# Optimization experiments

Hardware: AMD Instinct MI355X
Metric: run time of the kernel (lower is better)

Reference implementation:

```python
import jax, jax.numpy as jnp
import numpy as np

N_PTS = 500000
IN_DIM = 2
M_FOURIER = 32
J_WAVELET = 3
Q = 12
DEGREE = 3
N_CONTROL = 25
EMB_DIM = 2 * M_FOURIER + 2 * (2 ** J_WAVELET - 1)  # 78
LN_EPS = 1e-5


def make_open_uniform_knots(num_control, degree):
    n_knots = num_control + degree + 1  # 29
    if n_knots <= 2 * (degree + 1):
        return np.linspace(0.0, 1.0, n_knots).astype(np.float32)
    n_internal = n_knots - 2 * (degree + 1)
    internal = np.linspace(0.0, 1.0, n_internal + 2)[1:-1]
    return np.concatenate([np.zeros(degree + 1), internal, np.ones(degree + 1)]).astype(np.float32)

KNOTS = jnp.asarray(make_open_uniform_knots(N_CONTROL, DEGREE))


def bspline_basis(x, knots, degree, n_basis):
    # x: (M,) -> (M, n_basis); faithful (truncated) Cox-de-Boor as in source
    x = jnp.clip(x, knots[0], knots[-1])
    left = knots[:n_basis]
    right = knots[1:n_basis + 1]
    N = ((x[:, None] >= left) & (x[:, None] < right)).astype(x.dtype)
    last = ((x >= left[-1]) & (x <= right[-1])).astype(x.dtype)
    N = N.at[:, -1].set(last)
    for p in range(1, degree + 1):
        d1 = knots[p:p + n_basis] - knots[:n_basis]
        d2 = knots[p + 1:p + 1 + n_basis] - knots[1:1 + n_basis]
        c1 = jnp.where(d1 != 0, (x[:, None] - knots[:n_basis]) / jnp.where(d1 != 0, d1, 1.0), 0.0)
        c2 = jnp.where(d2 != 0, (knots[p + 1:p + 1 + n_basis] - x[:, None]) / jnp.where(d2 != 0, d2, 1.0), 0.0)
        N_shift = jnp.concatenate([N[:, 1:], jnp.zeros_like(N[:, :1])], axis=1)  # i+1 < n_basis guard
        N = c1 * N + c2 * N_shift
    return N


def wavelet_features_2d(z, J):
    x, t = z[:, 0], z[:, 1]
    feats = []
    for j in range(J):
        num_k = 2 ** j
        scale = max(0.5 / num_k, 0.001)
        centers = jnp.asarray([(k + 0.5) / num_k for k in range(num_k)], dtype=z.dtype)
        ux = x[:, None] - centers[None, :]
        ut = t[:, None] - centers[None, :]
        for u in (ux, ut):
            v = u / scale
            feats.append((1.0 - v * v) * jnp.exp(-0.5 * v * v))
    return jnp.concatenate(feats, axis=1)  # (N, 2*(2^J-1))


def setup_inputs() -> dict:
    key = jax.random.key(0)
    ks = jax.random.split(key, 6)
    xt = jax.random.uniform(ks[0], (N_PTS, IN_DIM), dtype=jnp.float32)
    B_fourier = jax.random.normal(ks[1], (M_FOURIER, IN_DIM), dtype=jnp.float32) * 1.0  # sigma_B
    ln_gamma = jnp.ones((EMB_DIM,), jnp.float32)
    ln_beta = jnp.zeros((EMB_DIM,), jnp.float32)
    W = jax.random.normal(ks[2], (Q, EMB_DIM), dtype=jnp.float32) * 0.05
    b_inner = jnp.zeros((Q,), jnp.float32)
    inner_scale = jnp.asarray(0.5, jnp.float32)
    coeffs = jax.random.normal(ks[3], (Q, N_CONTROL), dtype=jnp.float32) * 0.05
    a = jax.random.normal(ks[4], (Q, 1), dtype=jnp.float32) * 0.05
    b_out = jnp.zeros((1,), jnp.float32)
    return {"xt": xt, "B_fourier": B_fourier, "ln_gamma": ln_gamma, "ln_beta": ln_beta,
            "W": W, "b_inner": b_inner, "inner_scale": inner_scale, "coeffs": coeffs,
            "a": a, "b_out": b_out}


def reference(xt, B_fourier, ln_gamma, ln_beta, W, b_inner, inner_scale, coeffs, a, b_out):
    # Fourier features
    proj = (2.0 * np.pi) * (xt @ B_fourier.T)  # (N, M)
    scale = 1.0 / (np.sqrt(M_FOURIER) + 1e-12)
    F = jnp.concatenate([jnp.sin(proj) * scale, jnp.cos(proj) * scale], axis=1)
    # Wavelet features
    Wf = wavelet_features_2d(xt, J_WAVELET)
    emb = jnp.concatenate([F, Wf], axis=1)  # (N, 78)
    # LayerNorm
    mu = jnp.mean(emb, axis=-1, keepdims=True)
    var = jnp.mean(jnp.square(emb - mu), axis=-1, keepdims=True)
    emb = (emb - mu) / jnp.sqrt(var + LN_EPS) * ln_gamma + ln_beta
    # KAN B-spline core
    u_inner = emb @ W.T + b_inner  # (N, Q)
    s = 0.5 * (jnp.tanh(inner_scale * u_inner) + 1.0)
    B_flat = bspline_basis(s.reshape(-1), KNOTS, DEGREE, N_CONTROL)  # (N*Q, 25)
    B = B_flat.reshape(emb.shape[0], Q, N_CONTROL)
    phi = jnp.einsum('nqc,qc->nq', B, coeffs)
    u_out = phi @ a + b_out  # (N, 1)
    return u_out
```

## Files before the change

### kernel.cpp

```cpp
#include <hip/hip_runtime.h>
#include <hip/hip_bf16.h>
#include <math.h>

#define MF 32
#define EMB 78
#define NQ 12
#define NC 25
#define NSPAN 22
#define BLK 256
#define FSCALE 0.17677669529663688f

typedef __attribute__((ext_vector_type(8))) short short8;
typedef __attribute__((ext_vector_type(4))) float f32x4;

#define WS_A    0
#define WS_SGSB 768
#define WS_P    800

__device__ __forceinline__ float fast_rcp(float x) { return __builtin_amdgcn_rcpf(x); }
__device__ __forceinline__ float satf(float x) { return fminf(fmaxf(x, 0.0f), 1.0f); }

__device__ __forceinline__ unsigned pack2(float a, float b) {
    __hip_bfloat16 ha = __float2bfloat16(a), hb = __float2bfloat16(b);
    unsigned short ua, ub;
    __builtin_memcpy(&ua, &ha, 2); __builtin_memcpy(&ub, &hb, 2);
    return (unsigned)ua | ((unsigned)ub << 16);
}

__device__ __forceinline__ unsigned bfpair(float a, float b) {
    unsigned ua = __builtin_bit_cast(unsigned, a);
    unsigned ub = __builtin_bit_cast(unsigned, b);
    ua += 0x7fffu + ((ua >> 16) & 1u);
    ub += 0x7fffu + ((ub >> 16) & 1u);
    return (ua >> 16) | (ub & 0xffff0000u);
}

__device__ __forceinline__ float4 deboor4(float s, int ii) {
    const float c22 = 1.0f / 22.0f;
    float k_m2 = satf((float)(ii - 2) * c22);
    float k_m1 = satf((float)(ii - 1) * c22);
    float k_0  = satf((float)(ii)     * c22);
    float k_p1 = satf((float)(ii + 1) * c22);
    float k_p2 = satf((float)(ii + 2) * c22);
    float k_p3 = satf((float)(ii + 3) * c22);
    float l1 = s - k_0, l2 = s - k_m1, l3 = s - k_m2;
    float r1 = k_p1 - s, r2 = k_p2 - s, r3 = k_p3 - s;
    float t0 = fast_rcp(r1 + l1);
    float N0 = r1 * t0, N1 = l1 * t0;
    float ta = N0 * fast_rcp(r1 + l2);
    float tb = N1 * fast_rcp(r2 + l1);
    N0 = r1 * ta;
    N1 = fmaf(l2, ta, r2 * tb);
    float N2 = l1 * tb;
    float tc = N0 * fast_rcp(r1 + l3);
    float td = N1 * fast_rcp(r2 + l2);
    float te = N2 * fast_rcp(r3 + l1);
    N0 = r1 * tc;
    N1 = fmaf(l3, tc, r2 * td);
    N2 = fmaf(l2, td, r3 * te);
    float N3 = l1 * te;
    return make_float4(N0, N1, N2, N3);
}

__device__ __forceinline__ float wgf(const float* g, const float* W, int q, int k) {
    if (q >= NQ || k >= EMB) return 0.0f;
    float v = g[k] * W[q * EMB + k];
    return (k < 2 * MF) ? v * FSCALE : v;
}

__global__ __launch_bounds__(256) void pikan_setup(
    const float* __restrict__ g, const float* __restrict__ be,
    const float* __restrict__ W, const float* __restrict__ bi,
    const float* __restrict__ coeffs, const float* __restrict__ a,
    float* __restrict__ ws)
{
    const int tid = threadIdx.x;
    unsigned* wsu = (unsigned*)ws;

    for (int i = tid; i < 768; i += 256) {
        int d = i & 3, l = (i >> 2) & 63, kt = i >> 8;
        int q = l & 15;
        int kb = kt * 32 + (l >> 4) * 8 + d * 2;
        wsu[WS_A + i] = pack2(wgf(g, W, q, kb), wgf(g, W, q, kb + 1));
    }
    if (tid < 16) {
        float sg = 0.f, sb = 0.f;
        if (tid < NQ) {
            for (int e = 0; e < EMB; ++e) {
                float w = W[tid * EMB + e];
                sg += g[e] * w;
                sb += be[e] * w;
            }
            sb += bi[tid];
        }
        ws[WS_SGSB + 2 * tid]     = sg;
        ws[WS_SGSB + 2 * tid + 1] = sb;
    }
    for (int i = tid; i < 16 * NSPAN; i += 256) {
        int q = i / NSPAN, ii = i - q * NSPAN;
        float4 o = make_float4(0.f, 0.f, 0.f, 0.f);
        if (q < NQ) {
            float f[4];
            #pragma unroll
            for (int j = 0; j < 4; ++j) {
                float u = (float)j / 3.0f;
                float s = ((float)ii + u) * (1.0f / 22.0f);
                float4 N = deboor4(s, ii);
                const float* cq = coeffs + q * NC + ii;
                f[j] = N.x * cq[0] + N.y * cq[1] + N.z * cq[2] + N.w * cq[3];
            }
            float c0 = f[0];
            float c1 = -5.5f * f[0] +  9.0f * f[1] -  4.5f * f[2] +  1.0f * f[3];
            float c2 =  9.0f * f[0] - 22.5f * f[1] + 18.0f * f[2] -  4.5f * f[3];
            float c3 = -4.5f * f[0] + 13.5f * f[1] - 13.5f * f[2] +  4.5f * f[3];
            float aq = a[q];
            o = make_float4(c0 * aq, c1 * aq, c2 * aq, c3 * aq);
        }
        reinterpret_cast<float4*>(ws + WS_P)[i] = o;
    }
}

__global__ __launch_bounds__(BLK) __attribute__((amdgpu_waves_per_eu(4, 4)))
void pikan_main(
    const float* __restrict__ xt, const float* __restrict__ Bf,
    const float* __restrict__ isc_p, const float* __restrict__ bout_p,
    const float* __restrict__ ws, float* __restrict__ out, int npts)
{
    __shared__ uint4  sEmb[4][256];
    __shared__ float4 sPoly[16 * NSPAN];

    const int tid = threadIdx.x;
    for (int i = tid; i < 16 * NSPAN; i += BLK)
        sPoly[i] = reinterpret_cast<const float4*>(ws + WS_P)[i];
    __syncthreads();

    const int l = tid & 63, w = tid >> 6;
    const int g16 = l >> 4, c16 = l & 15;
    const int sw = (l >> 1) & 3;
    uint4* myEmb = sEmb[w];

    float sgq[4], sbq[4];
    #pragma unroll
    for (int r = 0; r < 4; ++r) {
        int q = g16 * 4 + r;
        sgq[r] = ws[WS_SGSB + 2 * q];
        sbq[r] = ws[WS_SGSB + 2 * q + 1];
    }
    const float kexp = -2.0f * isc_p[0] * 1.4426950408889634f;
    const float bout = bout_p[0];
    const int base = (blockIdx.x * 4 + w) * 128;

    #pragma unroll 1
    for (int pass = 0; pass < 2; ++pass) {
        const int pbase = base + pass * 64;
        const int pt = pbase + l;
        const bool valid = pt < npts;
        float x = 0.f, t = 0.f;
        if (valid) { float2 p = reinterpret_cast<const float2*>(xt)[pt]; x = p.x; t = p.y; }

        f32x4 acc[4];
        #pragma unroll
        for (int n = 0; n < 4; ++n) acc[n] = (f32x4){0.f, 0.f, 0.f, 0.f};

        auto stage = [&](uint4 a0, uint4 a1, uint4 a2, uint4 a3) {
            myEmb[l * 4 + (0 ^ sw)] = a0;
            myEmb[l * 4 + (1 ^ sw)] = a1;
            myEmb[l * 4 + (2 ^ sw)] = a2;
            myEmb[l * 4 + (3 ^ sw)] = a3;
        };
        auto mfma_kt = [&](int kt) {
            uint4 au = reinterpret_cast<const uint4*>(ws)[kt * 64 + l];
            short8 af = __builtin_bit_cast(short8, au);
            #pragma unroll
            for (int n = 0; n < 4; ++n) {
                int p = n * 16 + c16;
                uint4 bu = myEmb[p * 4 + (g16 ^ sw)];
                short8 bf = __builtin_bit_cast(short8, bu);
                acc[n] = __builtin_amdgcn_mfma_f32_16x16x32_bf16(af, bf, acc[n], 0, 0, 0);
            }
        };

        float sumf = 0.f, ssf = 0.f;
        unsigned spk[16], cpk[16];
        #pragma unroll
        for (int mp = 0; mp < 16; ++mp) {
            float rev0 = fmaf(x, Bf[4 * mp + 0], t * Bf[4 * mp + 1]);
            float rev1 = fmaf(x, Bf[4 * mp + 2], t * Bf[4 * mp + 3]);
#if __has_builtin(__builtin_amdgcn_fractf)
            float f0 = __builtin_amdgcn_fractf(rev0);
            float f1 = __builtin_amdgcn_fractf(rev1);
#else
            float f0 = rev0 - floorf(rev0);
            float f1 = rev1 - floorf(rev1);
#endif
            float s0 = __builtin_amdgcn_sinf(f0), s1 = __builtin_amdgcn_sinf(f1);
            float c0 = __builtin_amdgcn_cosf(f0), c1 = __builtin_amdgcn_cosf(f1);
            sumf += (s0 + s1) + (c0 + c1);
            ssf = fmaf(s0, s0, fmaf(s1, s1, fmaf(c0, c0, fmaf(c1, c1, ssf))));
            spk[mp] = bfpair(s0, s1);
            cpk[mp] = bfpair(c0, c1);
        }
        stage(make_uint4(spk[0], spk[1], spk[2],  spk[3]),
              make_uint4(spk[4], spk[5], spk[6],  spk[7]),
              make_uint4(spk[8], spk[9], spk[10], spk[11]),
              make_uint4(spk[12], spk[13], spk[14], spk[15]));
        mfma_kt(0);
        stage(make_uint4(cpk[0], cpk[1], cpk[2],  cpk[3]),
              make_uint4(cpk[4], cpk[5], cpk[6],  cpk[7]),
              make_uint4(cpk[8], cpk[9], cpk[10], cpk[11]),
              make_uint4(cpk[12], cpk[13], cpk[14], cpk[15]));
        mfma_kt(1);

        float w14[14];
        float sumw = 0.f, ssw = 0.f;
        {
            int o = 0;
            #pragma unroll
            for (int j = 0; j < 3; ++j) {
                const int nk = 1 << j;
                const float inv = (float)(2 * nk);
                #pragma unroll
                for (int k = 0; k < nk; ++k) {
                    float c = ((float)k + 0.5f) / (float)nk;
                    float v = (x - c) * inv, v2 = v * v;
                    float f = (1.0f - v2) * __expf(-0.5f * v2);
                    w14[o + k] = f; sumw += f; ssw = fmaf(f, f, ssw);
                }
                #pragma unroll
                for (int k = 0; k < nk; ++k) {
                    float c = ((float)k + 0.5f) / (float)nk;
                    float v = (t - c) * inv, v2 = v * v;
                    float f = (1.0f - v2) * __expf(-0.5f * v2);
                    w14[o + nk + k] = f; sumw += f; ssw = fmaf(f, f, ssw);
                }
                o += 2 * nk;
            }
        }
        stage(make_uint4(bfpair(w14[0], w14[1]), bfpair(w14[2], w14[3]),
                         bfpair(w14[4], w14[5]), bfpair(w14[6], w14[7])),
              make_uint4(bfpair(w14[8], w14[9]), bfpair(w14[10], w14[11]),
                         bfpair(w14[12], w14[13]), 0u),
              make_uint4(0u, 0u, 0u, 0u),
              make_uint4(0u, 0u, 0u, 0u));
        mfma_kt(2);

        const float sum = fmaf(FSCALE, sumf, sumw);
        const float ssq = fmaf(FSCALE * FSCALE, ssf, ssw);
        const float mu = sum * (1.0f / EMB);
        float var = fmaf(-mu, mu, ssq * (1.0f / EMB));
        var = fmaxf(var, 0.0f);
        const float istd = rsqrtf(var + 1e-5f);

        float yout = 0.f;
        #pragma unroll
        for (int n = 0; n < 4; ++n) {
            float mun  = __shfl(mu,   n * 16 + c16);
            float istn = __shfl(istd, n * 16 + c16);
            float yn = 0.f;
            #pragma unroll
            for (int r = 0; r < 4; ++r) {
                float uq = fmaf(istn, fmaf(-mun, sgq[r], acc[n][r]), sbq[r]);
                float e2 = __builtin_amdgcn_exp2f(kexp * uq);
                float s = fast_rcp(1.0f + e2);
                float v = s * 22.0f;
                int ii = (int)v; ii = ii > 21 ? 21 : ii;
                float uu = v - (float)ii;
                float4 cc = sPoly[(g16 * 4 + r) * NSPAN + ii];
                yn += fmaf(fmaf(fmaf(cc.w, uu, cc.z), uu, cc.y), uu, cc.x);
            }
            yn += __shfl_xor(yn, 16);
            yn += __shfl_xor(yn, 32);
            if (g16 == n) yout = yn;
        }
        if (valid) out[pt] = yout + bout;
    }
}

extern "C" void kernel_launch(void* const* d_in, const int* in_sizes, int n_in,
                              void* d_out, int out_size, void* d_ws, size_t ws_size,
                              hipStream_t stream) {
    const float* xt          = (const float*)d_in[0];
    const float* Bf          = (const float*)d_in[1];
    const float* gamma       = (const float*)d_in[2];
    const float* beta        = (const float*)d_in[3];
    const float* W           = (const float*)d_in[4];
    const float* b_inner     = (const float*)d_in[5];
    const float* inner_scale = (const float*)d_in[6];
    const float* coeffs      = (const float*)d_in[7];
    const float* a           = (const float*)d_in[8];
    const float* b_out       = (const float*)d_in[9];
    float* out = (float*)d_out;
    float* ws  = (float*)d_ws;

    const int npts = in_sizes[0] / 2;
    pikan_setup<<<1, 256, 0, stream>>>(gamma, beta, W, b_inner, coeffs, a, ws);
    const int grid = (npts + 511) / 512;
    pikan_main<<<grid, BLK, 0, stream>>>(xt, Bf, inner_scale, b_out, ws, out, npts);
}
```

Before: 27.64 us.

## Interleave sin/cos per frequency, use sin²+cos²=1 identity, one point per thread

Each thread now handles one point with 512-thread blocks and no two-pass loop, which raises the number of resident waves. Sin and cos of the same frequency are packed together, and the weight packing in setup is remapped to the new embedding order. The sum of squares of the Fourier features is replaced by the constant 32, using sin²+cos²=1, which removes the per-element FMAs. Occupancy hints change from waves_per_eu(4,4) to launch_bounds(512,8), which risks register pressure.

```diff
diff --git a/kernel.cpp b/kernel.cpp
--- a/kernel.cpp
+++ b/kernel.cpp
@@ -7,7 +7,8 @@
 #define NQ 12
 #define NC 25
 #define NSPAN 22
-#define BLK 256
+#define BLK 512
+#define NWAVE 8
 #define FSCALE 0.17677669529663688f
 
 typedef __attribute__((ext_vector_type(8))) short short8;
@@ -62,6 +63,14 @@
     return make_float4(N0, N1, N2, N3);
 }
 
+__device__ __forceinline__ int kmap(int kt, int kk) {
+    if (kt < 2) {
+        int m = kt * 16 + (kk >> 1);
+        return (kk & 1) ? (MF + m) : m;
+    }
+    return 64 + kk;
+}
+
 __device__ __forceinline__ float wgf(const float* g, const float* W, int q, int k) {
     if (q >= NQ || k >= EMB) return 0.0f;
     float v = g[k] * W[q * EMB + k];
@@ -80,8 +89,9 @@
     for (int i = tid; i < 768; i += 256) {
         int d = i & 3, l = (i >> 2) & 63, kt = i >> 8;
         int q = l & 15;
-        int kb = kt * 32 + (l >> 4) * 8 + d * 2;
-        wsu[WS_A + i] = pack2(wgf(g, W, q, kb), wgf(g, W, q, kb + 1));
+        int kk = (l >> 4) * 8 + d * 2;
+        wsu[WS_A + i] = pack2(wgf(g, W, q, kmap(kt, kk)),
+                              wgf(g, W, q, kmap(kt, kk + 1)));
     }
     if (tid < 16) {
         float sg = 0.f, sb = 0.f;
@@ -120,13 +130,12 @@
     }
 }
 
-__global__ __launch_bounds__(BLK) __attribute__((amdgpu_waves_per_eu(4, 4)))
-void pikan_main(
+__global__ __launch_bounds__(BLK, 8) void pikan_main(
     const float* __restrict__ xt, const float* __restrict__ Bf,
     const float* __restrict__ isc_p, const float* __restrict__ bout_p,
     const float* __restrict__ ws, float* __restrict__ out, int npts)
 {
-    __shared__ uint4  sEmb[4][256];
+    __shared__ uint4  sEmb[NWAVE][256];
     __shared__ float4 sPoly[16 * NSPAN];
 
     const int tid = threadIdx.x;
@@ -139,6 +148,93 @@
     const int sw = (l >> 1) & 3;
     uint4* myEmb = sEmb[w];
 
+    const int pt = blockIdx.x * BLK + tid;
+    const bool valid = pt < npts;
+    float x = 0.f, t = 0.f;
+    if (valid) { float2 p = reinterpret_cast<const float2*>(xt)[pt]; x = p.x; t = p.y; }
+
+    f32x4 acc[4];
+    #pragma unroll
+    for (int n = 0; n < 4; ++n) acc[n] = (f32x4){0.f, 0.f, 0.f, 0.f};
+
+    auto stW = [&](int d, uint4 v) { myEmb[l * 4 + (d ^ sw)] = v; };
+    auto mfma_kt = [&](int kt) {
+        uint4 au = reinterpret_cast<const uint4*>(ws)[kt * 64 + l];
+        short8 af = __builtin_bit_cast(short8, au);
+        #pragma unroll
+        for (int n = 0; n < 4; ++n) {
+            int p = n * 16 + c16;
+            uint4 bu = myEmb[p * 4 + (g16 ^ sw)];
+            short8 bf = __builtin_bit_cast(short8, bu);
+            acc[n] = __builtin_amdgcn_mfma_f32_16x16x32_bf16(af, bf, acc[n], 0, 0, 0);
+        }
+    };
+
+    float sumf = 0.f;
+    #pragma unroll
+    for (int kt = 0; kt < 2; ++kt) {
+        #pragma unroll
+        for (int d = 0; d < 4; ++d) {
+            unsigned dw[4];
+            #pragma unroll
+            for (int j = 0; j < 4; ++j) {
+                int m = kt * 16 + d * 4 + j;
+                float rev = fmaf(x, Bf[2 * m], t * Bf[2 * m + 1]);
+#if __has_builtin(__builtin_amdgcn_fractf)
+                float fr = __builtin_amdgcn_fractf(rev);
+#else
+                float fr = rev - floorf(rev);
+#endif
+                float s0 = __builtin_amdgcn_sinf(fr);
+                float c0 = __builtin_amdgcn_cosf(fr);
+                sumf += s0 + c0;
+                dw[j] = bfpair(s0, c0);
+            }
+            stW(d, make_uint4(dw[0], dw[1], dw[2], dw[3]));
+        }
+        mfma_kt(kt);
+    }
+
+    float w14[14];
+    float sumw = 0.f, ssw = 0.f;
+    {
+        int o = 0;
+        #pragma unroll
+        for (int j = 0; j < 3; ++j) {
+            const int nk = 1 << j;
+            const float inv = (float)(2 * nk);
+            #pragma unroll
+            for (int k = 0; k < nk; ++k) {
+                float c = ((float)k + 0.5f) / (float)nk;
+                float v = (x - c) * inv, v2 = v * v;
+                float f = (1.0f - v2) * __expf(-0.5f * v2);
+                w14[o + k] = f; sumw += f; ssw = fmaf(f, f, ssw);
+            }
+            #pragma unroll
+            for (int k = 0; k < nk; ++k) {
+                float c = ((float)k + 0.5f) / (float)nk;
+                float v = (t - c) * inv, v2 = v * v;
+                float f = (1.0f - v2) * __expf(-0.5f * v2);
+                w14[o + nk + k] = f; sumw += f; ssw = fmaf(f, f, ssw);
+            }
+            o += 2 * nk;
+        }
+    }
+    stW(0, make_uint4(bfpair(w14[0], w14[1]), bfpair(w14[2], w14[3]),
+                      bfpair(w14[4], w14[5]), bfpair(w14[6], w14[7])));
+    stW(1, make_uint4(bfpair(w14[8], w14[9]), bfpair(w14[10], w14[11]),
+                      bfpair(w14[12], w14[13]), 0u));
+    stW(2, make_uint4(0u, 0u, 0u, 0u));
+    stW(3, make_uint4(0u, 0u, 0u, 0u));
+    mfma_kt(2);
+
+    const float sum = fmaf(FSCALE, sumf, sumw);
+    const float ssq = fmaf(FSCALE * FSCALE, 32.0f, ssw);
+    const float mu = sum * (1.0f / EMB);
+    float var = fmaf(-mu, mu, ssq * (1.0f / EMB));
+    var = fmaxf(var, 0.0f);
+    const float istd = rsqrtf(var + 1e-5f);
+
     float sgq[4], sbq[4];
     #pragma unroll
     for (int r = 0; r < 4; ++r) {
@@ -148,132 +244,29 @@
     }
     const float kexp = -2.0f * isc_p[0] * 1.4426950408889634f;
     const float bout = bout_p[0];
-    const int base = (blockIdx.x * 4 + w) * 128;
-
-    #pragma unroll 1
-    for (int pass = 0; pass < 2; ++pass) {
-        const int pbase = base + pass * 64;
-        const int pt = pbase + l;
-        const bool valid = pt < npts;
-        float x = 0.f, t = 0.f;
-        if (valid) { float2 p = reinterpret_cast<const float2*>(xt)[pt]; x = p.x; t = p.y; }
-
-        f32x4 acc[4];
-        #pragma unroll
-        for (int n = 0; n < 4; ++n) acc[n] = (f32x4){0.f, 0.f, 0.f, 0.f};
-
-        auto stage = [&](uint4 a0, uint4 a1, uint4 a2, uint4 a3) {
-            myEmb[l * 4 + (0 ^ sw)] = a0;
-            myEmb[l * 4 + (1 ^ sw)] = a1;
-            myEmb[l * 4 + (2 ^ sw)] = a2;
-            myEmb[l * 4 + (3 ^ sw)] = a3;
-        };
-        auto mfma_kt = [&](int kt) {
-            uint4 au = reinterpret_cast<const uint4*>(ws)[kt * 64 + l];
-            short8 af = __builtin_bit_cast(short8, au);
-            #pragma unroll
-            for (int n = 0; n < 4; ++n) {
-                int p = n * 16 + c16;
-                uint4 bu = myEmb[p * 4 + (g16 ^ sw)];
-                short8 bf = __builtin_bit_cast(short8, bu);
-                acc[n] = __builtin_amdgcn_mfma_f32_16x16x32_bf16(af, bf, acc[n], 0, 0, 0);
-            }
-        };
-
-        float sumf = 0.f, ssf = 0.f;
-        unsigned spk[16], cpk[16];
-        #pragma unroll
-        for (int mp = 0; mp < 16; ++mp) {
-            float rev0 = fmaf(x, Bf[4 * mp + 0], t * Bf[4 * mp + 1]);
-            float rev1 = fmaf(x, Bf[4 * mp + 2], t * Bf[4 * mp + 3]);
-#if __has_builtin(__builtin_amdgcn_fractf)
-            float f0 = __builtin_amdgcn_fractf(rev0);
-            float f1 = __builtin_amdgcn_fractf(rev1);
-#else
-            float f0 = rev0 - floorf(rev0);
-            float f1 = rev1 - floorf(rev1);
-#endif
-            float s0 = __builtin_amdgcn_sinf(f0), s1 = __builtin_amdgcn_sinf(f1);
-            float c0 = __builtin_amdgcn_cosf(f0), c1 = __builtin_amdgcn_cosf(f1);
-            sumf += (s0 + s1) + (c0 + c1);
-            ssf = fmaf(s0, s0, fmaf(s1, s1, fmaf(c0, c0, fmaf(c1, c1, ssf))));
-            spk[mp] = bfpair(s0, s1);
-            cpk[mp] = bfpair(c0, c1);
-        }
-        stage(make_uint4(spk[0], spk[1], spk[2],  spk[3]),
-              make_uint4(spk[4], spk[5], spk[6],  spk[7]),
-              make_uint4(spk[8], spk[9], spk[10], spk[11]),
-              make_uint4(spk[12], spk[13], spk[14], spk[15]));
-        mfma_kt(0);
-        stage(make_uint4(cpk[0], cpk[1], cpk[2],  cpk[3]),
-              make_uint4(cpk[4], cpk[5], cpk[6],  cpk[7]),
-              make_uint4(cpk[8], cpk[9], cpk[10], cpk[11]),
-              make_uint4(cpk[12], cpk[13], cpk[14], cpk[15]));
-        mfma_kt(1);
-
-        float w14[14];
-        float sumw = 0.f, ssw = 0.f;
-        {
-            int o = 0;
-            #pragma unroll
-            for (int j = 0; j < 3; ++j) {
-                const int nk = 1 << j;
-                const float inv = (float)(2 * nk);
-                #pragma unroll
-                for (int k = 0; k < nk; ++k) {
-                    float c = ((float)k + 0.5f) / (float)nk;
-                    float v = (x - c) * inv, v2 = v * v;
-                    float f = (1.0f - v2) * __expf(-0.5f * v2);
-                    w14[o + k] = f; sumw += f; ssw = fmaf(f, f, ssw);
-                }
-                #pragma unroll
-                for (int k = 0; k < nk; ++k) {
-                    float c = ((float)k + 0.5f) / (float)nk;
-                    float v = (t - c) * inv, v2 = v * v;
-                    float f = (1.0f - v2) * __expf(-0.5f * v2);
-                    w14[o + nk + k] = f; sumw += f; ssw = fmaf(f, f, ssw);
-                }
-                o += 2 * nk;
-            }
-        }
-        stage(make_uint4(bfpair(w14[0], w14[1]), bfpair(w14[2], w14[3]),
-                         bfpair(w14[4], w14[5]), bfpair(w14[6], w14[7])),
-              make_uint4(bfpair(w14[8], w14[9]), bfpair(w14[10], w14[11]),
-                         bfpair(w14[12], w14[13]), 0u),
-              make_uint4(0u, 0u, 0u, 0u),
-              make_uint4(0u, 0u, 0u, 0u));
-        mfma_kt(2);
-
-        const float sum = fmaf(FSCALE, sumf, sumw);
-        const float ssq = fmaf(FSCALE * FSCALE, ssf, ssw);
-        const float mu = sum * (1.0f / EMB);
-        float var = fmaf(-mu, mu, ssq * (1.0f / EMB));
-        var = fmaxf(var, 0.0f);
-        const float istd = rsqrtf(var + 1e-5f);
-
-        float yout = 0.f;
-        #pragma unroll
-        for (int n = 0; n < 4; ++n) {
-            float mun  = __shfl(mu,   n * 16 + c16);
-            float istn = __shfl(istd, n * 16 + c16);
-            float yn = 0.f;
-            #pragma unroll
-            for (int r = 0; r < 4; ++r) {
-                float uq = fmaf(istn, fmaf(-mun, sgq[r], acc[n][r]), sbq[r]);
-                float e2 = __builtin_amdgcn_exp2f(kexp * uq);
-                float s = fast_rcp(1.0f + e2);
-                float v = s * 22.0f;
-                int ii = (int)v; ii = ii > 21 ? 21 : ii;
-                float uu = v - (float)ii;
-                float4 cc = sPoly[(g16 * 4 + r) * NSPAN + ii];
-                yn += fmaf(fmaf(fmaf(cc.w, uu, cc.z), uu, cc.y), uu, cc.x);
-            }
-            yn += __shfl_xor(yn, 16);
-            yn += __shfl_xor(yn, 32);
-            if (g16 == n) yout = yn;
-        }
-        if (valid) out[pt] = yout + bout;
-    }
+
+    float yout = 0.f;
+    #pragma unroll
+    for (int n = 0; n < 4; ++n) {
+        float mun  = __shfl(mu,   n * 16 + c16);
+        float istn = __shfl(istd, n * 16 + c16);
+        float yn = 0.f;
+        #pragma unroll
+        for (int r = 0; r < 4; ++r) {
+            float uq = fmaf(istn, fmaf(-mun, sgq[r], acc[n][r]), sbq[r]);
+            float e2 = __builtin_amdgcn_exp2f(kexp * uq);
+            float s = fast_rcp(1.0f + e2);
+            float v = s * 22.0f;
+            int ii = (int)v; ii = ii > 21 ? 21 : ii;
+            float uu = v - (float)ii;
+            float4 cc = sPoly[(g16 * 4 + r) * NSPAN + ii];
+            yn += fmaf(fmaf(fmaf(cc.w, uu, cc.z), uu, cc.y), uu, cc.x);
+        }
+        yn += __shfl_xor(yn, 16);
+        yn += __shfl_xor(yn, 32);
+        if (g16 == n) yout = yn;
+    }
+    if (valid) out[pt] = yout + bout;
 }
 
 extern "C" void kernel_launch(void* const* d_in, const int* in_sizes, int n_in,
@@ -294,6 +287,6 @@
 
     const int npts = in_sizes[0] / 2;
     pikan_setup<<<1, 256, 0, stream>>>(gamma, beta, W, b_inner, coeffs, a, ws);
-    const int grid = (npts + 511) / 512;
+    const int grid = (npts + BLK - 1) / BLK;
     pikan_main<<<grid, BLK, 0, stream>>>(xt, Bf, inner_scale, b_out, ws, out, npts);
 }
```

After: 26.09 us. 1.06x faster.
